# Kernel optimization log

Hardware: AMD Instinct MI355X
Metric: run time of the kernel (lower is better)

Reference implementation:

```python
import jax, jax.numpy as jnp
import numpy as np

B, S, E, H = 2, 2048, 1024, 16
DH = E // H  # 64


def setup_inputs() -> dict:
    key = jax.random.key(0)
    ks = jax.random.split(key, 9)
    sc = 1.0 / np.sqrt(E)
    return {
        "x": jax.random.normal(ks[0], (B, S, E), dtype=jnp.float32),
        "Wq": jax.random.normal(ks[1], (E, E), dtype=jnp.float32) * sc,
        "bq": jax.random.normal(ks[2], (E,), dtype=jnp.float32) * 0.02,
        "Wk": jax.random.normal(ks[3], (E, E), dtype=jnp.float32) * sc,
        "bk": jax.random.normal(ks[4], (E,), dtype=jnp.float32) * 0.02,
        "Wv": jax.random.normal(ks[5], (E, E), dtype=jnp.float32) * sc,
        "bv": jax.random.normal(ks[6], (E,), dtype=jnp.float32) * 0.02,
        "Wo": jax.random.normal(ks[7], (E, E), dtype=jnp.float32) * sc,
        "bo": jax.random.normal(ks[8], (E,), dtype=jnp.float32) * 0.02,
    }


def reference(x, Wq, bq, Wk, bk, Wv, bv, Wo, bo):
    b, s, e = x.shape
    h, dh = H, e // H
    # NOTE: original torch code does .view(B, H, S, Dh) on the [B, S, E]
    # projection WITHOUT transposing first; we replicate that exact reshape.
    q = (x @ Wq.T + bq).reshape(b, h, s, dh)
    k = (x @ Wk.T + bk).reshape(b, h, s, dh)
    v = (x @ Wv.T + bv).reshape(b, h, s, dh)
    scale = 1.0 / jnp.sqrt(jnp.asarray(dh, dtype=x.dtype))
    scores = jax.nn.softmax(jnp.einsum("bhqd,bhkd->bhqk", q, k) * scale, axis=-1)
    out = jnp.einsum("bhqk,bhkd->bhqd", scores, v)  # [B,H,S,Dh]
    out = out.transpose(0, 2, 1, 3).reshape(b, s, e)  # matches torch transpose(1,2).view
    return out @ Wo.T + bo
```

## Files before the change

### kernel.cpp

```cpp
#include <hip/hip_runtime.h>
#include <hip/hip_bf16.h>
#include <stdint.h>

typedef __bf16 bf16x8 __attribute__((ext_vector_type(8)));
typedef float  f32x4  __attribute__((ext_vector_type(4)));
typedef float  f32x16 __attribute__((ext_vector_type(16)));
typedef __hip_bfloat16 bf16;

__device__ __forceinline__ void gll16(const void* g, void* l) {
    typedef const unsigned int __attribute__((address_space(1)))* gp_t;
    typedef unsigned int __attribute__((address_space(3)))* lp_t;
    __builtin_amdgcn_global_load_lds((gp_t)(g), (lp_t)(l), 16, 0, 0);
}

__device__ __forceinline__ float fexp2(float x) {
#if __has_builtin(__builtin_amdgcn_exp2f)
    return __builtin_amdgcn_exp2f(x);
#else
    float r; asm volatile("v_exp_f32 %0, %1" : "=v"(r) : "v"(x)); return r;
#endif
}

__device__ __forceinline__ float tmax16(const f32x16& v) {
    float a0 = fmaxf(v[0], v[1]),   a1 = fmaxf(v[2], v[3]);
    float a2 = fmaxf(v[4], v[5]),   a3 = fmaxf(v[6], v[7]);
    float a4 = fmaxf(v[8], v[9]),   a5 = fmaxf(v[10], v[11]);
    float a6 = fmaxf(v[12], v[13]), a7 = fmaxf(v[14], v[15]);
    float b0 = fmaxf(a0, a1), b1 = fmaxf(a2, a3);
    float b2 = fmaxf(a4, a5), b3 = fmaxf(a6, a7);
    return fmaxf(fmaxf(b0, b1), fmaxf(b2, b3));
}
__device__ __forceinline__ float tsum16(const f32x16& v) {
    float a0 = v[0] + v[1],   a1 = v[2] + v[3];
    float a2 = v[4] + v[5],   a3 = v[6] + v[7];
    float a4 = v[8] + v[9],   a5 = v[10] + v[11];
    float a6 = v[12] + v[13], a7 = v[14] + v[15];
    float b0 = a0 + a1, b1 = a2 + a3, b2 = a4 + a5, b3 = a6 + a7;
    return (b0 + b1) + (b2 + b3);
}

__global__ __launch_bounds__(256) void prep_convert(
    const float* __restrict__ x,
    const float* __restrict__ wq, const float* __restrict__ wk,
    const float* __restrict__ wv, const float* __restrict__ wo,
    bf16* __restrict__ Xb, bf16* __restrict__ Wcat, bf16* __restrict__ Wob)
{
    int i = blockIdx.x * blockDim.x + threadIdx.x;
    int base = i * 4;
    const float* src; bf16* dst;
    if      (base < 4194304) { src = x  + base;             dst = Xb   + base; }
    else if (base < 5242880) { src = wq + (base - 4194304); dst = Wcat + (base - 4194304); }
    else if (base < 6291456) { src = wk + (base - 5242880); dst = Wcat + 1048576 + (base - 5242880); }
    else if (base < 7340032) { src = wv + (base - 6291456); dst = Wcat + 2097152 + (base - 6291456); }
    else                     { src = wo + (base - 7340032); dst = Wob  + (base - 7340032); }
    float4 v = *(const float4*)src;
    union { bf16 h[4]; ushort4 u; } cv;
    cv.h[0] = __float2bfloat16(v.x);
    cv.h[1] = __float2bfloat16(v.y);
    cv.h[2] = __float2bfloat16(v.z);
    cv.h[3] = __float2bfloat16(v.w);
    *(ushort4*)dst = cv.u;
}

__global__ __launch_bounds__(256, 2) void gemm_qkv(
    const bf16* __restrict__ X, const bf16* __restrict__ Wc,
    const float* __restrict__ bq, const float* __restrict__ bk, const float* __restrict__ bv,
    bf16* __restrict__ Pq, bf16* __restrict__ Pk, bf16* __restrict__ Pv)
{
    __shared__ __align__(16) bf16 Ab[128 * 32];
    __shared__ __align__(16) bf16 Bb[128 * 32];
    const int id = blockIdx.x;
    const int sid = (id & 7) * 96 + (id >> 3);
    const int t = threadIdx.x;
    const int lane = t & 63, w = t >> 6;
    const int lr = lane & 15, lg = lane >> 4;
    const int wr = w >> 1, wc = w & 1;
    const int row0 = (sid / 24) * 128, col0 = (sid % 24) * 128;

    f32x4 acc[4][4] = {};

    const char* Xc  = (const char*)X;
    const char* Wcc = (const char*)Wc;
    char* AbC = (char*)Ab;
    char* BbC = (char*)Bb;
    const int o0 = t * 16, o1 = o0 + 4096;
    const int ldsoff = w * 1024;

    for (int k0 = 0; k0 < 1024; k0 += 32) {
        __syncthreads();
        gll16(Xc  + (size_t)(row0 + (o0 >> 6)) * 2048 + (size_t)k0 * 2 + (o0 & 63), AbC + ldsoff);
        gll16(Wcc + (size_t)(col0 + (o0 >> 6)) * 2048 + (size_t)k0 * 2 + (o0 & 63), BbC + ldsoff);
        gll16(Xc  + (size_t)(row0 + (o1 >> 6)) * 2048 + (size_t)k0 * 2 + (o1 & 63), AbC + 4096 + ldsoff);
        gll16(Wcc + (size_t)(col0 + (o1 >> 6)) * 2048 + (size_t)k0 * 2 + (o1 & 63), BbC + 4096 + ldsoff);
        __syncthreads();
        bf16x8 af[4], bw[4];
        #pragma unroll
        for (int i = 0; i < 4; ++i)
            af[i] = *(const bf16x8*)(AbC + ((wr * 64 + i * 16 + lr) * 32 + lg * 8) * 2);
        #pragma unroll
        for (int j = 0; j < 4; ++j)
            bw[j] = *(const bf16x8*)(BbC + ((wc * 64 + j * 16 + lr) * 32 + lg * 8) * 2);
        #pragma unroll
        for (int i = 0; i < 4; ++i)
            #pragma unroll
            for (int j = 0; j < 4; ++j)
                acc[i][j] = __builtin_amdgcn_mfma_f32_16x16x32_bf16(af[i], bw[j], acc[i][j], 0, 0, 0);
    }

    const int mid = col0 >> 10;
    const float* bias = (mid == 0) ? bq : (mid == 1 ? bk : bv);
    bf16* Out = (mid == 0) ? Pq : (mid == 1 ? Pk : Pv);
    const float scale = (mid == 0) ? 0.125f * 1.44269504f : 1.0f;
    const int nc0 = col0 - (mid << 10) + wc * 64;
    const int mr0 = row0 + wr * 64;
    #pragma unroll
    for (int i = 0; i < 4; ++i)
        #pragma unroll
        for (int j = 0; j < 4; ++j) {
            int cc = nc0 + j * 16 + lr;
            float bsv = bias[cc];
            #pragma unroll
            for (int p = 0; p < 4; ++p) {
                int rr = mr0 + i * 16 + lg * 4 + p;
                Out[(size_t)rr * 1024 + cc] = __float2bfloat16((acc[i][j][p] + bsv) * scale);
            }
        }
}

__global__ __launch_bounds__(256) void transpose_v(const bf16* __restrict__ Pv, bf16* __restrict__ Vt)
{
    __shared__ bf16 tile[64][72];
    const int head = blockIdx.y;
    const int st   = blockIdx.x;
    const bf16* src = Pv + (size_t)head * 131072 + (size_t)st * 4096;
    bf16* dst = Vt + (size_t)head * 131072 + (size_t)st * 64;
    const int t = threadIdx.x;
    const int rr = t >> 2, c0 = (t & 3) * 16;
    #pragma unroll
    for (int u = 0; u < 2; ++u) {
        bf16x8 v = *(const bf16x8*)(src + rr * 64 + c0 + u * 8);
        #pragma unroll
        for (int e = 0; e < 8; ++e) tile[rr][c0 + u * 8 + e] = ((const bf16*)&v)[e];
    }
    __syncthreads();
    #pragma unroll
    for (int u = 0; u < 2; ++u) {
        bf16 ov[8];
        #pragma unroll
        for (int e = 0; e < 8; ++e) {
            int y = u * 8 + e;
            int z = (y & 3) | ((y & 8) >> 1) | ((y & 4) << 1);
            ov[e] = tile[c0 + z][rr];
        }
        *(bf16x8*)(dst + (size_t)rr * 2048 + c0 + u * 8) = *(const bf16x8*)ov;
    }
}

__global__ __launch_bounds__(256, 2) void attn_fwd(
    const bf16* __restrict__ Pq, const bf16* __restrict__ Pk,
    const bf16* __restrict__ Vt, bf16* __restrict__ Of)
{
    __shared__ __align__(16) bf16 Kl[2][128 * 64];
    __shared__ __align__(16) bf16 Vl[2][64 * 128];

    const int blk0 = blockIdx.x;
    const int blk = (blk0 & 7) * 64 + (blk0 >> 3);
    const int head = blk >> 4;
    const int qt = blk & 15;
    const int bb = head >> 4, hh = head & 15;
    const bf16* Qh = Pq + (size_t)head * 131072;
    const char* Khc = (const char*)(Pk + (size_t)head * 131072);
    const char* Vhc = (const char*)(Vt + (size_t)head * 131072);

    const int t = threadIdx.x;
    const int lane = t & 63, w = t >> 6;
    const int ql = lane & 31, hi = lane >> 5;
    const int q0 = qt * 128 + w * 32;

    bf16x8 qf[4];
    #pragma unroll
    for (int m = 0; m < 4; ++m)
        qf[m] = *(const bf16x8*)(Qh + (size_t)(q0 + ql) * 64 + m * 16 + hi * 8);

    f32x16 acc[2] = {};
    float m_run = -1e30f, l_run = 0.f;

    const int stg_o   = t * 16;
    const int stg_key = stg_o >> 7, stg_ks = (stg_o >> 4) & 7;
    const int stg_d   = stg_o >> 8, stg_vs = (stg_o >> 4) & 15;
    const size_t kgo = (size_t)stg_key * 128 + ((stg_ks ^ (stg_key & 7)) * 16);
    const size_t vgo = (size_t)stg_d * 4096 + ((stg_vs ^ (stg_d & 7)) * 16);
    const int ldst = w * 1024;

#define STAGE(S0, BUF)                                                          \
    {                                                                           \
        char* KB = (char*)(Kl[BUF]);                                            \
        char* VB = (char*)(Vl[BUF]);                                            \
        _Pragma("unroll")                                                       \
        for (int qq = 0; qq < 4; ++qq) {                                        \
            gll16(Khc + (size_t)(S0) * 128 + (size_t)qq * 4096 + kgo,           \
                  KB + qq * 4096 + ldst);                                       \
            gll16(Vhc + (size_t)(S0) * 2 + (size_t)qq * 65536 + vgo,            \
                  VB + qq * 4096 + ldst);                                       \
        }                                                                       \
    }

    STAGE(0, 0);
    __syncthreads();

    int cur = 0;
    for (int s0 = 0; s0 < 2048; s0 += 128) {
        if (s0 + 128 < 2048) STAGE(s0 + 128, cur ^ 1);

        const char* KlC = (const char*)(Kl[cur]);
        const char* VlC = (const char*)(Vl[cur]);

        f32x16 sa[4] = {};
        __builtin_amdgcn_s_setprio(1);
        #pragma unroll
        for (int kb = 0; kb < 4; ++kb) {
            int row = kb * 32 + ql;
            #pragma unroll
            for (int m = 0; m < 4; ++m) {
                int byt = row * 128 + ((32 * m + 16 * hi) ^ ((row & 7) << 4));
                bf16x8 kf = *(const bf16x8*)(KlC + byt);
                sa[kb] = __builtin_amdgcn_mfma_f32_32x32x16_bf16(kf, qf[m], sa[kb], 0, 0, 0);
            }
        }
        __builtin_amdgcn_s_setprio(0);

        float mx = fmaxf(fmaxf(tmax16(sa[0]), tmax16(sa[1])),
                         fmaxf(tmax16(sa[2]), tmax16(sa[3])));
        mx = fmaxf(mx, __shfl_xor(mx, 32));

        float mn;
        if (__all(mx - m_run <= 8.0f)) {
            mn = m_run;
        } else {
            mn = fmaxf(m_run, mx);
            float al = fexp2(m_run - mn);
            m_run = mn;
            l_run *= al;
            #pragma unroll
            for (int r = 0; r < 16; ++r) { acc[0][r] *= al; acc[1][r] *= al; }
        }

        #pragma unroll
        for (int kb = 0; kb < 4; ++kb)
            #pragma unroll
            for (int r = 0; r < 16; ++r)
                sa[kb][r] = fexp2(sa[kb][r] - mn);
        float rs = (tsum16(sa[0]) + tsum16(sa[1])) + (tsum16(sa[2]) + tsum16(sa[3]));
        rs += __shfl_xor(rs, 32);
        l_run += rs;

        __builtin_amdgcn_s_setprio(1);
        #pragma unroll
        for (int sb = 0; sb < 8; ++sb) {
            const int kb = sb >> 1, par = (sb & 1) * 8;
            bf16x8 pa;
            #pragma unroll
            for (int e = 0; e < 8; ++e) pa[e] = (__bf16)sa[kb][par + e];
            #pragma unroll
            for (int db = 0; db < 2; ++db) {
                int row = db * 32 + ql;
                int byt = row * 256 + ((sb * 32 + hi * 16) ^ ((row & 7) << 4));
                bf16x8 vf = *(const bf16x8*)(VlC + byt);
                acc[db] = __builtin_amdgcn_mfma_f32_32x32x16_bf16(vf, pa, acc[db], 0, 0, 0);
            }
        }
        __builtin_amdgcn_s_setprio(0);

        __syncthreads();
        cur ^= 1;
    }
#undef STAGE

    float inv = 1.0f / l_run;
    bf16* orow = Of + (size_t)(bb * 2048 + q0 + ql) * 1024 + hh * 64;
    #pragma unroll
    for (int db = 0; db < 2; ++db)
        #pragma unroll
        for (int g = 0; g < 4; ++g) {
            union { bf16 h[4]; ushort4 u; } ob;
            #pragma unroll
            for (int j = 0; j < 4; ++j)
                ob.h[j] = __float2bfloat16(acc[db][4 * g + j] * inv);
            *(ushort4*)(orow + db * 32 + 8 * g + 4 * hi) = ob.u;
        }
}

__global__ __launch_bounds__(256, 2) void gemm_out(
    const bf16* __restrict__ A, const bf16* __restrict__ W,
    const float* __restrict__ bo, float* __restrict__ C)
{
    __shared__ __align__(16) bf16 Ab[128 * 32];
    __shared__ __align__(16) bf16 Bb[128 * 32];
    const int id = blockIdx.x;
    const int sid = (id & 7) * 32 + (id >> 3);
    const int t = threadIdx.x;
    const int lane = t & 63, w = t >> 6;
    const int lr = lane & 15, lg = lane >> 4;
    const int wr = w >> 1, wc = w & 1;
    const int row0 = (sid / 8) * 128, col0 = (sid % 8) * 128;

    f32x4 acc[4][4] = {};
    const char* Ac = (const char*)A;
    const char* Wc = (const char*)W;
    char* AbC = (char*)Ab;
    char* BbC = (char*)Bb;
    const int o0 = t * 16, o1 = o0 + 4096;
    const int ldsoff = w * 1024;

    for (int k0 = 0; k0 < 1024; k0 += 32) {
        __syncthreads();
        gll16(Ac + (size_t)(row0 + (o0 >> 6)) * 2048 + (size_t)k0 * 2 + (o0 & 63), AbC + ldsoff);
        gll16(Wc + (size_t)(col0 + (o0 >> 6)) * 2048 + (size_t)k0 * 2 + (o0 & 63), BbC + ldsoff);
        gll16(Ac + (size_t)(row0 + (o1 >> 6)) * 2048 + (size_t)k0 * 2 + (o1 & 63), AbC + 4096 + ldsoff);
        gll16(Wc + (size_t)(col0 + (o1 >> 6)) * 2048 + (size_t)k0 * 2 + (o1 & 63), BbC + 4096 + ldsoff);
        __syncthreads();
        bf16x8 af[4], bw[4];
        #pragma unroll
        for (int i = 0; i < 4; ++i)
            af[i] = *(const bf16x8*)(AbC + ((wr * 64 + i * 16 + lr) * 32 + lg * 8) * 2);
        #pragma unroll
        for (int j = 0; j < 4; ++j)
            bw[j] = *(const bf16x8*)(BbC + ((wc * 64 + j * 16 + lr) * 32 + lg * 8) * 2);
        #pragma unroll
        for (int i = 0; i < 4; ++i)
            #pragma unroll
            for (int j = 0; j < 4; ++j)
                acc[i][j] = __builtin_amdgcn_mfma_f32_16x16x32_bf16(af[i], bw[j], acc[i][j], 0, 0, 0);
    }

    const int nc0 = col0 + wc * 64;
    const int mr0 = row0 + wr * 64;
    #pragma unroll
    for (int i = 0; i < 4; ++i)
        #pragma unroll
        for (int j = 0; j < 4; ++j) {
            int cc = nc0 + j * 16 + lr;
            float bsv = bo[cc];
            #pragma unroll
            for (int p = 0; p < 4; ++p) {
                int rr = mr0 + i * 16 + lg * 4 + p;
                C[(size_t)rr * 1024 + cc] = acc[i][j][p] + bsv;
            }
        }
}

extern "C" void kernel_launch(void* const* d_in, const int* in_sizes, int n_in,
                              void* d_out, int out_size, void* d_ws, size_t ws_size,
                              hipStream_t stream) {
    const float* x  = (const float*)d_in[0];
    const float* Wq = (const float*)d_in[1];
    const float* bq = (const float*)d_in[2];
    const float* Wk = (const float*)d_in[3];
    const float* bk = (const float*)d_in[4];
    const float* Wv = (const float*)d_in[5];
    const float* bv = (const float*)d_in[6];
    const float* Wo = (const float*)d_in[7];
    const float* bo = (const float*)d_in[8];
    float* out = (float*)d_out;

    char* ws = (char*)d_ws;
    bf16* Xb   = (bf16*)(ws + 0);
    bf16* Wcat = (bf16*)(ws + 8388608);
    bf16* Wob  = (bf16*)(ws + 14680064);
    bf16* Pq   = (bf16*)(ws + 16777216);
    bf16* Pk   = (bf16*)(ws + 25165824);
    bf16* Pv   = (bf16*)(ws + 33554432);
    bf16* Vt   = (bf16*)(ws + 0);
    bf16* Of   = (bf16*)(ws + 33554432);
    (void)ws_size; (void)in_sizes; (void)n_in; (void)out_size;

    prep_convert<<<8192, 256, 0, stream>>>(x, Wq, Wk, Wv, Wo, Xb, Wcat, Wob);
    gemm_qkv<<<768, 256, 0, stream>>>(Xb, Wcat, bq, bk, bv, Pq, Pk, Pv);
    transpose_v<<<dim3(32, 32), 256, 0, stream>>>(Pv, Vt);
    attn_fwd<<<512, 256, 0, stream>>>(Pq, Pk, Vt, Of);
    gemm_out<<<256, 256, 0, stream>>>(Of, Wob, bo, out);
}
```

Measured before the change: 123.5 us.

## Compute V transposed directly via GEMM and load V fragments from global in attention

```diff
diff --git a/kernel.cpp b/kernel.cpp
--- a/kernel.cpp
+++ b/kernel.cpp
@@ -62,20 +62,20 @@
     *(ushort4*)dst = cv.u;
 }
 
-__global__ __launch_bounds__(256, 2) void gemm_qkv(
+__global__ __launch_bounds__(256, 2) void gemm_qk(
     const bf16* __restrict__ X, const bf16* __restrict__ Wc,
-    const float* __restrict__ bq, const float* __restrict__ bk, const float* __restrict__ bv,
-    bf16* __restrict__ Pq, bf16* __restrict__ Pk, bf16* __restrict__ Pv)
+    const float* __restrict__ bq, const float* __restrict__ bk,
+    bf16* __restrict__ Pq, bf16* __restrict__ Pk)
 {
     __shared__ __align__(16) bf16 Ab[128 * 32];
     __shared__ __align__(16) bf16 Bb[128 * 32];
     const int id = blockIdx.x;
-    const int sid = (id & 7) * 96 + (id >> 3);
+    const int sid = (id & 7) * 64 + (id >> 3);
     const int t = threadIdx.x;
     const int lane = t & 63, w = t >> 6;
     const int lr = lane & 15, lg = lane >> 4;
     const int wr = w >> 1, wc = w & 1;
-    const int row0 = (sid / 24) * 128, col0 = (sid % 24) * 128;
+    const int row0 = (sid >> 4) * 128, col0 = (sid & 15) * 128;
 
     f32x4 acc[4][4] = {};
 
@@ -108,8 +108,8 @@
     }
 
     const int mid = col0 >> 10;
-    const float* bias = (mid == 0) ? bq : (mid == 1 ? bk : bv);
-    bf16* Out = (mid == 0) ? Pq : (mid == 1 ? Pk : Pv);
+    const float* bias = (mid == 0) ? bq : bk;
+    bf16* Out = (mid == 0) ? Pq : Pk;
     const float scale = (mid == 0) ? 0.125f * 1.44269504f : 1.0f;
     const int nc0 = col0 - (mid << 10) + wc * 64;
     const int mr0 = row0 + wr * 64;
@@ -127,33 +127,69 @@
         }
 }
 
-__global__ __launch_bounds__(256) void transpose_v(const bf16* __restrict__ Pv, bf16* __restrict__ Vt)
+__global__ __launch_bounds__(256, 2) void gemm_vt(
+    const bf16* __restrict__ Wv, const bf16* __restrict__ X,
+    const float* __restrict__ bv, bf16* __restrict__ Vt)
 {
-    __shared__ bf16 tile[64][72];
-    const int head = blockIdx.y;
-    const int st   = blockIdx.x;
-    const bf16* src = Pv + (size_t)head * 131072 + (size_t)st * 4096;
-    bf16* dst = Vt + (size_t)head * 131072 + (size_t)st * 64;
+    __shared__ __align__(16) bf16 Ab[128 * 32];
+    __shared__ __align__(16) bf16 Bb[128 * 32];
+    const int id = blockIdx.x;
+    const int sid = (id & 7) * 32 + (id >> 3);
     const int t = threadIdx.x;
-    const int rr = t >> 2, c0 = (t & 3) * 16;
+    const int lane = t & 63, w = t >> 6;
+    const int lr = lane & 15, lg = lane >> 4;
+    const int wr = w >> 1, wc = w & 1;
+    const int row0 = (sid >> 5) * 128, col0 = (sid & 31) * 128;
+
+    f32x4 acc[4][4] = {};
+    const char* Ac = (const char*)Wv;
+    const char* Bc = (const char*)X;
+    char* AbC = (char*)Ab;
+    char* BbC = (char*)Bb;
+    const int o0 = t * 16, o1 = o0 + 4096;
+    const int ldsoff = w * 1024;
+
+    for (int k0 = 0; k0 < 1024; k0 += 32) {
+        __syncthreads();
+        gll16(Ac + (size_t)(row0 + (o0 >> 6)) * 2048 + (size_t)k0 * 2 + (o0 & 63), AbC + ldsoff);
+        gll16(Bc + (size_t)(col0 + (o0 >> 6)) * 2048 + (size_t)k0 * 2 + (o0 & 63), BbC + ldsoff);
+        gll16(Ac + (size_t)(row0 + (o1 >> 6)) * 2048 + (size_t)k0 * 2 + (o1 & 63), AbC + 4096 + ldsoff);
+        gll16(Bc + (size_t)(col0 + (o1 >> 6)) * 2048 + (size_t)k0 * 2 + (o1 & 63), BbC + 4096 + ldsoff);
+        __syncthreads();
+        bf16x8 af[4], bw[4];
+        #pragma unroll
+        for (int i = 0; i < 4; ++i)
+            af[i] = *(const bf16x8*)(AbC + ((wr * 64 + i * 16 + lr) * 32 + lg * 8) * 2);
+        #pragma unroll
+        for (int j = 0; j < 4; ++j)
+            bw[j] = *(const bf16x8*)(BbC + ((wc * 64 + j * 16 + lr) * 32 + lg * 8) * 2);
+        #pragma unroll
+        for (int i = 0; i < 4; ++i)
+            #pragma unroll
+            for (int j = 0; j < 4; ++j)
+                acc[i][j] = __builtin_amdgcn_mfma_f32_16x16x32_bf16(af[i], bw[j], acc[i][j], 0, 0, 0);
+    }
+
+    const int nc0 = col0 + wc * 64;
+    const int mr0 = row0 + wr * 64;
     #pragma unroll
-    for (int u = 0; u < 2; ++u) {
-        bf16x8 v = *(const bf16x8*)(src + rr * 64 + c0 + u * 8);
-        #pragma unroll
-        for (int e = 0; e < 8; ++e) tile[rr][c0 + u * 8 + e] = ((const bf16*)&v)[e];
-    }
-    __syncthreads();
-    #pragma unroll
-    for (int u = 0; u < 2; ++u) {
-        bf16 ov[8];
-        #pragma unroll
-        for (int e = 0; e < 8; ++e) {
-            int y = u * 8 + e;
-            int z = (y & 3) | ((y & 8) >> 1) | ((y & 4) << 1);
-            ov[e] = tile[c0 + z][rr];
-        }
-        *(bf16x8*)(dst + (size_t)rr * 2048 + c0 + u * 8) = *(const bf16x8*)ov;
-    }
+    for (int i = 0; i < 4; ++i)
+        #pragma unroll
+        for (int j = 0; j < 4; ++j) {
+            int cc = nc0 + j * 16 + lr;
+            int head = (cc >> 11) * 16 + ((cc >> 7) & 15);
+            int rc   = cc & 127;
+            #pragma unroll
+            for (int p = 0; p < 4; ++p) {
+                int rr = mr0 + i * 16 + lg * 4 + p;
+                int s4 = (rr >> 6) & 15;
+                int s4x = (s4 & 3) | ((s4 & 4) << 1) | ((s4 & 8) >> 1);
+                int d  = rr & 63;
+                float vv = acc[i][j][p] + bv[rr];
+                Vt[(size_t)head * 131072 + (size_t)d * 2048 + rc * 16 + s4x]
+                    = __float2bfloat16(vv);
+            }
+        }
 }
 
 __global__ __launch_bounds__(256, 2) void attn_fwd(
@@ -161,7 +197,6 @@
     const bf16* __restrict__ Vt, bf16* __restrict__ Of)
 {
     __shared__ __align__(16) bf16 Kl[2][128 * 64];
-    __shared__ __align__(16) bf16 Vl[2][64 * 128];
 
     const int blk0 = blockIdx.x;
     const int blk = (blk0 & 7) * 64 + (blk0 >> 3);
@@ -187,33 +222,35 @@
 
     const int stg_o   = t * 16;
     const int stg_key = stg_o >> 7, stg_ks = (stg_o >> 4) & 7;
-    const int stg_d   = stg_o >> 8, stg_vs = (stg_o >> 4) & 15;
     const size_t kgo = (size_t)stg_key * 128 + ((stg_ks ^ (stg_key & 7)) * 16);
-    const size_t vgo = (size_t)stg_d * 4096 + ((stg_vs ^ (stg_d & 7)) * 16);
     const int ldst = w * 1024;
 
-#define STAGE(S0, BUF)                                                          \
+#define KSTAGE(S0, BUF)                                                         \
     {                                                                           \
         char* KB = (char*)(Kl[BUF]);                                            \
-        char* VB = (char*)(Vl[BUF]);                                            \
         _Pragma("unroll")                                                       \
-        for (int qq = 0; qq < 4; ++qq) {                                        \
+        for (int qq = 0; qq < 4; ++qq)                                          \
             gll16(Khc + (size_t)(S0) * 128 + (size_t)qq * 4096 + kgo,           \
                   KB + qq * 4096 + ldst);                                       \
-            gll16(Vhc + (size_t)(S0) * 2 + (size_t)qq * 65536 + vgo,            \
-                  VB + qq * 4096 + ldst);                                       \
-        }                                                                       \
     }
 
-    STAGE(0, 0);
+    const char* vrow0 = Vhc + (size_t)ql * 4096 + hi * 16;
+    const char* vrow1 = Vhc + (size_t)(32 + ql) * 4096 + hi * 16;
+
+    KSTAGE(0, 0);
     __syncthreads();
 
     int cur = 0;
     for (int s0 = 0; s0 < 2048; s0 += 128) {
-        if (s0 + 128 < 2048) STAGE(s0 + 128, cur ^ 1);
+        bf16x8 v0[8], v1[8];
+        #pragma unroll
+        for (int sb = 0; sb < 8; ++sb) {
+            v0[sb] = *(const bf16x8*)(vrow0 + (size_t)s0 * 2 + sb * 32);
+            v1[sb] = *(const bf16x8*)(vrow1 + (size_t)s0 * 2 + sb * 32);
+        }
+        if (s0 + 128 < 2048) KSTAGE(s0 + 128, cur ^ 1);
 
         const char* KlC = (const char*)(Kl[cur]);
-        const char* VlC = (const char*)(Vl[cur]);
 
         f32x16 sa[4] = {};
         __builtin_amdgcn_s_setprio(1);
@@ -261,20 +298,15 @@
             bf16x8 pa;
             #pragma unroll
             for (int e = 0; e < 8; ++e) pa[e] = (__bf16)sa[kb][par + e];
-            #pragma unroll
-            for (int db = 0; db < 2; ++db) {
-                int row = db * 32 + ql;
-                int byt = row * 256 + ((sb * 32 + hi * 16) ^ ((row & 7) << 4));
-                bf16x8 vf = *(const bf16x8*)(VlC + byt);
-                acc[db] = __builtin_amdgcn_mfma_f32_32x32x16_bf16(vf, pa, acc[db], 0, 0, 0);
-            }
+            acc[0] = __builtin_amdgcn_mfma_f32_32x32x16_bf16(v0[sb], pa, acc[0], 0, 0, 0);
+            acc[1] = __builtin_amdgcn_mfma_f32_32x32x16_bf16(v1[sb], pa, acc[1], 0, 0, 0);
         }
         __builtin_amdgcn_s_setprio(0);
 
         __syncthreads();
         cur ^= 1;
     }
-#undef STAGE
+#undef KSTAGE
 
     float inv = 1.0f / l_run;
     bf16* orow = Of + (size_t)(bb * 2048 + q0 + ql) * 1024 + hh * 64;
@@ -369,14 +401,13 @@
     bf16* Wob  = (bf16*)(ws + 14680064);
     bf16* Pq   = (bf16*)(ws + 16777216);
     bf16* Pk   = (bf16*)(ws + 25165824);
-    bf16* Pv   = (bf16*)(ws + 33554432);
-    bf16* Vt   = (bf16*)(ws + 0);
-    bf16* Of   = (bf16*)(ws + 33554432);
+    bf16* Vt   = (bf16*)(ws + 33554432);
+    bf16* Of   = (bf16*)(ws + 0);
     (void)ws_size; (void)in_sizes; (void)n_in; (void)out_size;
 
     prep_convert<<<8192, 256, 0, stream>>>(x, Wq, Wk, Wv, Wo, Xb, Wcat, Wob);
-    gemm_qkv<<<768, 256, 0, stream>>>(Xb, Wcat, bq, bk, bv, Pq, Pk, Pv);
-    transpose_v<<<dim3(32, 32), 256, 0, stream>>>(Pv, Vt);
+    gemm_qk<<<512, 256, 0, stream>>>(Xb, Wcat, bq, bk, Pq, Pk);
+    gemm_vt<<<256, 256, 0, stream>>>(Wcat + 2097152, Xb, bv, Vt);
     attn_fwd<<<512, 256, 0, stream>>>(Pq, Pk, Vt, Of);
     gemm_out<<<256, 256, 0, stream>>>(Of, Wob, bo, out);
 }
```

Result: slower. 170.0 us (+37.7%).
